# Kernel optimization log

Hardware: AMD Instinct MI355X
Metric: run time of the kernel (lower is better)

The kernel has to match this reference:

```python
import jax, jax.numpy as jnp
import numpy as np

NUM_HEADS = 4
EPS = 1e-12  # torch F.normalize eps


def _l2norm(t):
    # normalize along last axis, matching torch.nn.functional.normalize
    n = jnp.sqrt(jnp.sum(t * t, axis=-1, keepdims=True))
    return t / jnp.maximum(n, EPS)


def setup_inputs() -> dict:
    key = jax.random.key(0)
    k1, k2 = jax.random.split(key)
    B, N, C = 4, 8192, 768
    x = jax.random.normal(k1, (B, N, C), dtype=jnp.float32)
    W_qkvv = jax.random.normal(k2, (3 * C, C), dtype=jnp.float32) * (C ** -0.5)
    temperature = jnp.ones((NUM_HEADS, 1, 1), dtype=jnp.float32)
    return {"x": x, "W_qkvv": W_qkvv, "temperature": temperature}


def reference(x, W_qkvv, temperature):
    B, N, C = x.shape
    H = NUM_HEADS
    D = C // H
    # qkvv projection: [B,N,3C] -> [3,B,H,N,D]
    qkvv = (x @ W_qkvv.T).reshape(B, N, 3, H, D).transpose(2, 0, 3, 1, 4)
    q, k, v = qkvv[0], qkvv[1], qkvv[2]        # each [B,H,N,D]
    q = jnp.swapaxes(q, -2, -1)                # [B,H,D,N]
    k = jnp.swapaxes(k, -2, -1)                # [B,H,D,N]
    v = jnp.swapaxes(v, -2, -1)                # [B,H,D,N]
    q = _l2norm(q)
    k = _l2norm(k)
    # channel attention scores: [B,H,D,D], temperature broadcast per head
    attn = jnp.einsum('bhdn,bhen->bhde', q, k) * temperature[None]
    attn = jax.nn.softmax(attn, axis=-1)
    # dropout is identity in eval mode
    x_CA = jnp.einsum('bhde,bhen->bhdn', attn, v)   # [B,H,D,N]
    out = x_CA.transpose(0, 3, 1, 2).reshape(B, N, C)
    return out
```

## Files before the change

kernel.cpp:

```cpp
#include <hip/hip_runtime.h>
#include <hip/hip_bf16.h>
#include <cstddef>
#include <cstdint>

#define B_   4
#define N_   8192
#define C_   768
#define H_   4
#define D_   192
#define CQ_  2304
#define M_   32768

typedef __attribute__((ext_vector_type(8))) short short8_t;
typedef __attribute__((ext_vector_type(4))) float f32x4;

typedef const __attribute__((address_space(1))) uint gq_uint;
typedef __attribute__((address_space(3))) uint lds_uint;

__device__ inline ushort f2bf(float f){
  uint u = __float_as_uint(f);
  u += 0x7FFFu + ((u >> 16) & 1u);
  return (ushort)(u >> 16);
}
__device__ inline float bf2f(ushort u){ return __uint_as_float(((uint)u) << 16); }

__global__ __launch_bounds__(256) void cvt_bf16(const float* __restrict__ src,
                                                ushort* __restrict__ dst, int n4){
  int i = blockIdx.x * 256 + threadIdx.x;
  if (i < n4){
    float4 v = ((const float4*)src)[i];
    ushort4 o;
    o.x = f2bf(v.x); o.y = f2bf(v.y); o.z = f2bf(v.z); o.w = f2bf(v.w);
    ((ushort4*)dst)[i] = o;
  }
}

__global__ __launch_bounds__(512, 2) void gemm_qkvv(const ushort* __restrict__ A,
                                                    const ushort* __restrict__ W,
                                                    ushort* __restrict__ Cq,
                                                    float* __restrict__ norm2){
  extern __shared__ ushort lds[];
  const int t = threadIdx.x;
  const int bid = blockIdx.x;
  const int wg  = (bid & 7) * 144 + (bid >> 3);
  const int by = wg / 9, bx = wg % 9;
  const int m0 = by * 256, n0 = bx * 256;
  const int wid = t >> 6, lane = t & 63;
  const int wm = wid >> 2, wn = wid & 3;
  const int lr = lane & 15, lg = lane >> 4;
  const int srow  = lane >> 3;
  const int sslot = (lane & 7) ^ srow;

  f32x4 acc[8][4];
  #pragma unroll
  for (int i = 0; i < 8; ++i)
    #pragma unroll
    for (int j = 0; j < 4; ++j)
      acc[i][j] = (f32x4){0.f, 0.f, 0.f, 0.f};

  #define STAGE_HALF(GPTR, G0, KT, LBASE, HALF)                                 \
    do {                                                                        \
      _Pragma("unroll")                                                         \
      for (int rnd_ = 0; rnd_ < 2; ++rnd_){                                     \
        const int row_ = (HALF) * 128 + rnd_ * 64 + wid * 8;                    \
        __builtin_amdgcn_global_load_lds(                                       \
            (gq_uint*)(const void*)((GPTR) + (size_t)((G0) + row_ + srow) * 768 \
                                    + (KT) * 64 + sslot * 8),                   \
            (lds_uint*)(void*)((LBASE) + row_ * 64), 16, 0, 0);                 \
      }                                                                         \
    } while (0)

  #define RD_A(DST, MH)                                                         \
    _Pragma("unroll") for (int kk = 0; kk < 2; ++kk){                           \
      const int sl = ((kk * 4 + lg) ^ (lr & 7)) * 8;                            \
      _Pragma("unroll") for (int fm = 0; fm < 4; ++fm)                          \
        DST[kk][fm] = *(const short8_t*)(bA + ((MH)*128 + wm*64 + fm*16 + lr)*64 + sl); }

  #define RD_B(DST, NH)                                                         \
    _Pragma("unroll") for (int kk = 0; kk < 2; ++kk){                           \
      const int sl = ((kk * 4 + lg) ^ (lr & 7)) * 8;                            \
      _Pragma("unroll") for (int fl = 0; fl < 2; ++fl)                          \
        DST[kk][fl] = *(const short8_t*)(bB + ((NH)*128 + wn*32 + fl*16 + lr)*64 + sl); }

  #define MM(AR, BR, IO, JO)                                                    \
    __builtin_amdgcn_s_setprio(1);                                              \
    _Pragma("unroll") for (int kk = 0; kk < 2; ++kk)                            \
    _Pragma("unroll") for (int fm = 0; fm < 4; ++fm)                            \
    _Pragma("unroll") for (int fl = 0; fl < 2; ++fl)                            \
      acc[(IO)+fm][(JO)+fl] = __builtin_amdgcn_mfma_f32_16x16x32_bf16(          \
          AR[kk][fm], BR[kk][fl], acc[(IO)+fm][(JO)+fl], 0, 0, 0);              \
    __builtin_amdgcn_s_setprio(0);

  #define WAITP(N)                                                              \
    asm volatile("s_waitcnt vmcnt(" #N ")" ::: "memory");                       \
    __builtin_amdgcn_s_barrier();                                               \
    asm volatile("s_waitcnt lgkmcnt(0)" ::: "memory");                          \
    __builtin_amdgcn_sched_barrier(0);

  STAGE_HALF(A, m0, 0, lds,         0);
  STAGE_HALF(A, m0, 0, lds,         1);
  STAGE_HALF(W, n0, 0, lds + 16384, 0);
  STAGE_HALF(W, n0, 0, lds + 16384, 1);
  asm volatile("s_waitcnt vmcnt(0)" ::: "memory");
  __builtin_amdgcn_s_barrier();
  __builtin_amdgcn_sched_barrier(0);

  short8_t a0[2][4], a1[2][4], bf0[2][2], bf1[2][2];

  #pragma unroll 2
  for (int kt = 0; kt < 11; ++kt){
    const ushort* bA = lds + (kt & 1) * 32768;
    const ushort* bB = bA + 16384;
    ushort* nA = lds + ((kt + 1) & 1) * 32768;
    ushort* nB = nA + 16384;
    RD_A(a0, 0); RD_B(bf0, 0);
    STAGE_HALF(A, m0, kt + 1, nA, 0);
    WAITP(4);
    MM(a0, bf0, 0, 0);
    RD_A(a1, 1);
    STAGE_HALF(W, n0, kt + 1, nB, 0);
    WAITP(4);
    MM(a1, bf0, 4, 0);
    RD_B(bf1, 1);
    STAGE_HALF(A, m0, kt + 1, nA, 1);
    WAITP(4);
    MM(a1, bf1, 4, 2);
    STAGE_HALF(W, n0, kt + 1, nB, 1);
    WAITP(4);
    MM(a0, bf1, 0, 2);
  }
  {
    const ushort* bA = lds + 32768;
    const ushort* bB = bA + 16384;
    RD_A(a0, 0); RD_B(bf0, 0);
    WAITP(2);
    MM(a0, bf0, 0, 0);
    RD_A(a1, 1);
    WAITP(0);
    MM(a1, bf0, 4, 0);
    RD_B(bf1, 1);
    asm volatile("s_waitcnt lgkmcnt(0)" ::: "memory");
    __builtin_amdgcn_sched_barrier(0);
    MM(a1, bf1, 4, 2);
    MM(a0, bf1, 0, 2);
  }
  #undef STAGE_HALF
  #undef RD_A
  #undef RD_B
  #undef MM
  #undef WAITP

  #pragma unroll
  for (int i = 0; i < 8; ++i)
    #pragma unroll
    for (int j = 0; j < 4; ++j)
      #pragma unroll
      for (int r = 0; r < 4; ++r){
        int m = m0 + (i >> 2) * 128 + wm * 64 + (i & 3) * 16 + lg * 4 + r;
        int c = n0 + (j >> 1) * 128 + wn * 32 + (j & 1) * 16 + lr;
        Cq[(size_t)m * CQ_ + c] = f2bf(acc[i][j][r]);
      }

  if (bx < 6){
    const int b = m0 >> 13;
    #pragma unroll
    for (int j = 0; j < 4; ++j){
      float s = 0.f;
      #pragma unroll
      for (int i = 0; i < 8; ++i)
        #pragma unroll
        for (int r = 0; r < 4; ++r)
          s = fmaf(acc[i][j][r], acc[i][j][r], s);
      s += __shfl_xor(s, 16);
      s += __shfl_xor(s, 32);
      if (lg == 0)
        atomicAdd(&norm2[b * 1536 + n0 + (j >> 1) * 128 + wn * 32 + (j & 1) * 16 + lr], s);
    }
  }
}

__global__ __launch_bounds__(512) void gram_mfma(const ushort* __restrict__ Qk,
                                                 float* __restrict__ Sp){
  const int kc = blockIdx.x;
  const int bh = blockIdx.y;
  const int b = bh >> 2, h = bh & 3;
  __shared__ __align__(16) uint pk[2][2][3232];
  const int t = threadIdx.x;
  const int wid = t >> 6, lane = t & 63;
  const int wd = wid >> 2, we = wid & 3;
  const int lr = lane & 15, lg = lane >> 4;

  f32x4 acc[6][3];
  #pragma unroll
  for (int i = 0; i < 6; ++i)
    #pragma unroll
    for (int j = 0; j < 3; ++j)
      acc[i][j] = (f32x4){0.f, 0.f, 0.f, 0.f};

  const uint* gq = (const uint*)Qk + (size_t)b * N_ * 1152;

  uint r0[6], r1[6];
  #define GLOAD(IT)                                                             \
    _Pragma("unroll") for (int u = 0; u < 6; ++u){                              \
      int id = u*512 + t, mat = id/1536, rem = id - mat*1536;                   \
      int np = rem/96, c = rem - np*96;                                         \
      const uint* p = gq + (size_t)(kc*512 + (IT)*32 + 2*np)*1152               \
                         + (mat ? 384 + h*96 : h*96) + c;                       \
      r0[u] = p[0]; r1[u] = p[1152];                                            \
    }
  #define LWRITE(BUF)                                                           \
    _Pragma("unroll") for (int u = 0; u < 6; ++u){                              \
      int id = u*512 + t, mat = id/1536, rem = id - mat*1536;                   \
      int np = rem/96, c = rem - np*96;                                         \
      uint o0 = (r0[u] & 0xFFFFu) | (r1[u] << 16);                              \
      uint o1 = (r0[u] >> 16) | (r1[u] & 0xFFFF0000u);                          \
      *(uint2*)&pk[BUF][mat][np*202 + 2*c] = (uint2){o0, o1};                   \
    }

  GLOAD(0);
  LWRITE(0);
  __syncthreads();

  for (int it = 0; it < 16; ++it){
    const int cur = it & 1;
    if (it < 15) GLOAD(it + 1);
    union { uint u[4]; short8_t v; } af[6], bf[3];
    #pragma unroll
    for (int i = 0; i < 6; ++i){
      int d = wd * 96 + i * 16 + lr;
      #pragma unroll
      for (int p = 0; p < 4; ++p)
        af[i].u[p] = pk[cur][0][(lg*4 + p)*202 + d];
    }
    #pragma unroll
    for (int j = 0; j < 3; ++j){
      int e = we * 48 + j * 16 + lr;
      #pragma unroll
      for (int p = 0; p < 4; ++p)
        bf[j].u[p] = pk[cur][1][(lg*4 + p)*202 + e];
    }
    #pragma unroll
    for (int i = 0; i < 6; ++i)
      #pragma unroll
      for (int j = 0; j < 3; ++j)
        acc[i][j] = __builtin_amdgcn_mfma_f32_16x16x32_bf16(af[i].v, bf[j].v, acc[i][j], 0, 0, 0);
    if (it < 15) LWRITE(cur ^ 1);
    __syncthreads();
  }
  #undef GLOAD
  #undef LWRITE

  float* base = Sp + (size_t)(kc * 16 + bh) * 192 * 192;
  #pragma unroll
  for (int i = 0; i < 6; ++i)
    #pragma unroll
    for (int j = 0; j < 3; ++j)
      #pragma unroll
      for (int r = 0; r < 4; ++r){
        int d = wd * 96 + i * 16 + lg * 4 + r;
        int e = we * 48 + j * 16 + lr;
        base[(size_t)d * 192 + e] = acc[i][j][r];
      }
}

__global__ __launch_bounds__(256) void softmax_k(const float* __restrict__ Sp,
                                                 const float* __restrict__ norm2,
                                                 const float* __restrict__ temp,
                                                 ushort* __restrict__ attn){
  const int wid  = blockIdx.x * 4 + (threadIdx.x >> 6);
  const int lane = threadIdx.x & 63;
  const int bh = wid / 192, d = wid % 192;
  const int b = bh >> 2, h = bh & 3;
  const float nq = sqrtf(norm2[b*1536 + h*192 + d]);
  const float sc = temp[h] / fmaxf(nq, 1e-12f);
  const float* Sr = Sp + ((size_t)bh * 192 + d) * 192;
  float l[3];
  #pragma unroll
  for (int u = 0; u < 3; ++u){
    int e = lane + u * 64;
    float s = 0.f;
    #pragma unroll
    for (int kc = 0; kc < 16; ++kc)
      s += Sr[(size_t)kc * (16*192*192) + e];
    float nk = sqrtf(norm2[b*1536 + 768 + h*192 + e]);
    l[u] = s * sc / fmaxf(nk, 1e-12f);
  }
  float m = fmaxf(l[0], fmaxf(l[1], l[2]));
  #pragma unroll
  for (int off = 32; off; off >>= 1) m = fmaxf(m, __shfl_xor(m, off));
  float p[3], s = 0.f;
  #pragma unroll
  for (int u = 0; u < 3; ++u){ p[u] = expf(l[u] - m); s += p[u]; }
  #pragma unroll
  for (int off = 32; off; off >>= 1) s += __shfl_xor(s, off);
  float inv = 1.f / s;
  ushort* ar = attn + ((size_t)bh * 192 + d) * 192;
  #pragma unroll
  for (int u = 0; u < 3; ++u) ar[lane + u*64] = f2bf(p[u] * inv);
}

__global__ __launch_bounds__(256) void out_gemm(const ushort* __restrict__ Q,
                                                const ushort* __restrict__ attn,
                                                float* __restrict__ out){
  const int bh = blockIdx.y;
  const int b = bh >> 2, h = bh & 3;
  const int n0 = blockIdx.x * 128;
  const int t = threadIdx.x, w = t >> 6, lane = t & 63;
  const int wn = w & 1, wd = w >> 1;
  const int lr = lane & 15, lg = lane >> 4;
  f32x4 acc[4][6];
  #pragma unroll
  for (int i = 0; i < 4; ++i)
    #pragma unroll
    for (int j = 0; j < 6; ++j)
      acc[i][j] = (f32x4){0.f, 0.f, 0.f, 0.f};

  const ushort* Vbase = Q + 1536 + h * 192;
  const ushort* Abase = attn + (size_t)bh * 192 * 192;

  #pragma unroll
  for (int kk = 0; kk < 6; ++kk){
    const int e = kk * 32 + lg * 8;
    short8_t av[4], bv[6];
    #pragma unroll
    for (int f = 0; f < 4; ++f){
      int n = n0 + wn*64 + f*16 + lr;
      av[f] = *(const short8_t*)(Vbase + (size_t)(b*N_ + n) * CQ_ + e);
    }
    #pragma unroll
    for (int f = 0; f < 6; ++f){
      int d = wd*96 + f*16 + lr;
      bv[f] = *(const short8_t*)(Abase + d * 192 + e);
    }
    #pragma unroll
    for (int i = 0; i < 4; ++i)
      #pragma unroll
      for (int j = 0; j < 6; ++j)
        acc[i][j] = __builtin_amdgcn_mfma_f32_16x16x32_bf16(av[i], bv[j], acc[i][j], 0, 0, 0);
  }
  #pragma unroll
  for (int i = 0; i < 4; ++i)
    #pragma unroll
    for (int j = 0; j < 6; ++j)
      #pragma unroll
      for (int r = 0; r < 4; ++r){
        int n = n0 + wn*64 + i*16 + lg*4 + r;
        int c = h*192 + wd*96 + j*16 + lr;
        out[(size_t)(b*N_ + n) * 768 + c] = acc[i][j][r];
      }
}

extern "C" void kernel_launch(void* const* d_in, const int* in_sizes, int n_in,
                              void* d_out, int out_size, void* d_ws, size_t ws_size,
                              hipStream_t stream){
  const float* x    = (const float*)d_in[0];
  const float* Wq   = (const float*)d_in[1];
  const float* temp = (const float*)d_in[2];
  float* out = (float*)d_out;
  char* ws = (char*)d_ws;

  ushort* xb    = (ushort*)(ws + 0);
  float*  S_part= (float*)(ws + 0);
  ushort* attn  = (ushort*)(ws + 37748736);
  ushort* Wb    = (ushort*)(ws + 50331648);
  ushort* qkvv  = (ushort*)(ws + 53870592);
  float*  norm2 = (float*)(ws + 204865536);

  static_assert(sizeof(ushort) == 2, "");
  hipFuncSetAttribute((const void*)gemm_qkvv,
                      hipFuncAttributeMaxDynamicSharedMemorySize, 131072);

  hipMemsetAsync(norm2, 0, 24576, stream);

  cvt_bf16<<<6291456/256, 256, 0, stream>>>(x,  xb, 6291456);
  cvt_bf16<<<442368/256,  256, 0, stream>>>(Wq, Wb, 442368);

  gemm_qkvv<<<1152, 512, 131072, stream>>>(xb, Wb, qkvv, norm2);

  gram_mfma<<<dim3(16, 16), 512, 0, stream>>>(qkvv, S_part);
  softmax_k<<<768, 256, 0, stream>>>(S_part, norm2, temp, attn);
  out_gemm<<<dim3(64, 16), 256, 0, stream>>>(qkvv, attn, out);
}
```

Before: 239.1 us.

## Fuse fp32-to-bf16 conversion of x into the QKV GEMM A-tile staging

The separate pass that converted x to bf16 is removed. The QKV GEMM now loads fp32 x tiles into registers, packs them to bf16 with v_cvt_pk_bf16_f32, and writes them into LDS, while the weight tile still uses direct global-to-LDS loads. The norm2 memset is folded into the weight conversion kernel. This saves a full read and write of the converted x buffer and two launches. In exchange the GEMM's A-tile traffic doubles, register pressure rises, and the pipeline is restructured with new wait counts and barriers.

New measurement: 431.1 us. 1.8x slower.

```diff
diff --git a/kernel.cpp b/kernel.cpp
--- a/kernel.cpp
+++ b/kernel.cpp
@@ -25,8 +25,10 @@
 __device__ inline float bf2f(ushort u){ return __uint_as_float(((uint)u) << 16); }
 
 __global__ __launch_bounds__(256) void cvt_bf16(const float* __restrict__ src,
-                                                ushort* __restrict__ dst, int n4){
+                                                ushort* __restrict__ dst, int n4,
+                                                float* __restrict__ zbuf, int zn){
   int i = blockIdx.x * 256 + threadIdx.x;
+  if (i < zn) zbuf[i] = 0.f;
   if (i < n4){
     float4 v = ((const float4*)src)[i];
     ushort4 o;
@@ -35,7 +37,7 @@
   }
 }
 
-__global__ __launch_bounds__(512, 2) void gemm_qkvv(const ushort* __restrict__ A,
+__global__ __launch_bounds__(512, 2) void gemm_qkvv(const float* __restrict__ X,
                                                     const ushort* __restrict__ W,
                                                     ushort* __restrict__ Cq,
                                                     float* __restrict__ norm2){
@@ -58,13 +60,34 @@
     for (int j = 0; j < 4; ++j)
       acc[i][j] = (f32x4){0.f, 0.f, 0.f, 0.f};
 
-  #define STAGE_HALF(GPTR, G0, KT, LBASE, HALF)                                 \
+  #define ISSUE_A(RG, KT, HALF)                                                 \
+    _Pragma("unroll")                                                           \
+    for (int rnd_ = 0; rnd_ < 2; ++rnd_){                                       \
+      const int row_ = (HALF) * 128 + rnd_ * 64 + wid * 8 + srow;               \
+      const float* p_ = X + (size_t)(m0 + row_) * 768 + (KT) * 64 + sslot * 8;  \
+      RG[rnd_][0] = *(const float4*)p_;                                         \
+      RG[rnd_][1] = *(const float4*)(p_ + 4);                                   \
+    }
+
+  #define WRITE_A(RG, LBASE, HALF)                                              \
+    _Pragma("unroll")                                                           \
+    for (int rnd_ = 0; rnd_ < 2; ++rnd_){                                       \
+      uint q0_, q1_, q2_, q3_;                                                  \
+      asm("v_cvt_pk_bf16_f32 %0, %1, %2" : "=v"(q0_) : "v"(RG[rnd_][0].x), "v"(RG[rnd_][0].y)); \
+      asm("v_cvt_pk_bf16_f32 %0, %1, %2" : "=v"(q1_) : "v"(RG[rnd_][0].z), "v"(RG[rnd_][0].w)); \
+      asm("v_cvt_pk_bf16_f32 %0, %1, %2" : "=v"(q2_) : "v"(RG[rnd_][1].x), "v"(RG[rnd_][1].y)); \
+      asm("v_cvt_pk_bf16_f32 %0, %1, %2" : "=v"(q3_) : "v"(RG[rnd_][1].z), "v"(RG[rnd_][1].w)); \
+      const int row_ = (HALF) * 128 + rnd_ * 64 + wid * 8 + srow;               \
+      *(uint4*)((LBASE) + row_ * 64 + (lane & 7) * 8) = (uint4){q0_, q1_, q2_, q3_}; \
+    }
+
+  #define STAGE_W(KT, LBASE, HALF)                                              \
     do {                                                                        \
       _Pragma("unroll")                                                         \
       for (int rnd_ = 0; rnd_ < 2; ++rnd_){                                     \
         const int row_ = (HALF) * 128 + rnd_ * 64 + wid * 8;                    \
         __builtin_amdgcn_global_load_lds(                                       \
-            (gq_uint*)(const void*)((GPTR) + (size_t)((G0) + row_ + srow) * 768 \
+            (gq_uint*)(const void*)(W + (size_t)(n0 + row_ + srow) * 768        \
                                     + (KT) * 64 + sslot * 8),                   \
             (lds_uint*)(void*)((LBASE) + row_ * 64), 16, 0, 0);                 \
       }                                                                         \
@@ -91,21 +114,23 @@
           AR[kk][fm], BR[kk][fl], acc[(IO)+fm][(JO)+fl], 0, 0, 0);              \
     __builtin_amdgcn_s_setprio(0);
 
-  #define WAITP(N)                                                              \
-    asm volatile("s_waitcnt vmcnt(" #N ")" ::: "memory");                       \
+  #define BARRIER_LG                                                            \
     __builtin_amdgcn_s_barrier();                                               \
     asm volatile("s_waitcnt lgkmcnt(0)" ::: "memory");                          \
     __builtin_amdgcn_sched_barrier(0);
 
-  STAGE_HALF(A, m0, 0, lds,         0);
-  STAGE_HALF(A, m0, 0, lds,         1);
-  STAGE_HALF(W, n0, 0, lds + 16384, 0);
-  STAGE_HALF(W, n0, 0, lds + 16384, 1);
-  asm volatile("s_waitcnt vmcnt(0)" ::: "memory");
+  float4 fA0[2][2], fA1[2][2];
+  short8_t a0[2][4], a1[2][4], bf0[2][2], bf1[2][2];
+
+  ISSUE_A(fA0, 0, 0);
+  ISSUE_A(fA1, 0, 1);
+  STAGE_W(0, lds + 16384, 0);
+  STAGE_W(0, lds + 16384, 1);
+  WRITE_A(fA0, lds, 0);
+  WRITE_A(fA1, lds, 1);
+  asm volatile("s_waitcnt vmcnt(0) lgkmcnt(0)" ::: "memory");
   __builtin_amdgcn_s_barrier();
   __builtin_amdgcn_sched_barrier(0);
-
-  short8_t a0[2][4], a1[2][4], bf0[2][2], bf1[2][2];
 
   #pragma unroll 2
   for (int kt = 0; kt < 11; ++kt){
@@ -113,30 +138,41 @@
     const ushort* bB = bA + 16384;
     ushort* nA = lds + ((kt + 1) & 1) * 32768;
     ushort* nB = nA + 16384;
+
     RD_A(a0, 0); RD_B(bf0, 0);
-    STAGE_HALF(A, m0, kt + 1, nA, 0);
-    WAITP(4);
+    ISSUE_A(fA0, kt + 1, 0);
+    STAGE_W(kt + 1, nB, 0);
+    BARRIER_LG;
     MM(a0, bf0, 0, 0);
+
     RD_A(a1, 1);
-    STAGE_HALF(W, n0, kt + 1, nB, 0);
-    WAITP(4);
+    ISSUE_A(fA1, kt + 1, 1);
+    STAGE_W(kt + 1, nB, 1);
+    asm volatile("s_waitcnt vmcnt(12)" ::: "memory");
+    BARRIER_LG;
     MM(a1, bf0, 4, 0);
+
     RD_B(bf1, 1);
-    STAGE_HALF(A, m0, kt + 1, nA, 1);
-    WAITP(4);
+    WRITE_A(fA0, nA, 0);
+    BARRIER_LG;
     MM(a1, bf1, 4, 2);
-    STAGE_HALF(W, n0, kt + 1, nB, 1);
-    WAITP(4);
+
+    WRITE_A(fA1, nA, 1);
     MM(a0, bf1, 0, 2);
-  }
+    asm volatile("s_waitcnt lgkmcnt(0)" ::: "memory");
+    __builtin_amdgcn_s_barrier();
+    __builtin_amdgcn_sched_barrier(0);
+  }
+
   {
     const ushort* bA = lds + 32768;
     const ushort* bB = bA + 16384;
     RD_A(a0, 0); RD_B(bf0, 0);
-    WAITP(2);
+    BARRIER_LG;
     MM(a0, bf0, 0, 0);
     RD_A(a1, 1);
-    WAITP(0);
+    asm volatile("s_waitcnt vmcnt(0)" ::: "memory");
+    BARRIER_LG;
     MM(a1, bf0, 4, 0);
     RD_B(bf1, 1);
     asm volatile("s_waitcnt lgkmcnt(0)" ::: "memory");
@@ -144,11 +180,13 @@
     MM(a1, bf1, 4, 2);
     MM(a0, bf1, 0, 2);
   }
-  #undef STAGE_HALF
+  #undef ISSUE_A
+  #undef WRITE_A
+  #undef STAGE_W
   #undef RD_A
   #undef RD_B
   #undef MM
-  #undef WAITP
+  #undef BARRIER_LG
 
   #pragma unroll
   for (int i = 0; i < 8; ++i)
@@ -359,7 +397,6 @@
   float* out = (float*)d_out;
   char* ws = (char*)d_ws;
 
-  ushort* xb    = (ushort*)(ws + 0);
   float*  S_part= (float*)(ws + 0);
   ushort* attn  = (ushort*)(ws + 37748736);
   ushort* Wb    = (ushort*)(ws + 50331648);
@@ -370,12 +407,9 @@
   hipFuncSetAttribute((const void*)gemm_qkvv,
                       hipFuncAttributeMaxDynamicSharedMemorySize, 131072);
 
-  hipMemsetAsync(norm2, 0, 24576, stream);
-
-  cvt_bf16<<<6291456/256, 256, 0, stream>>>(x,  xb, 6291456);
-  cvt_bf16<<<442368/256,  256, 0, stream>>>(Wq, Wb, 442368);
-
-  gemm_qkvv<<<1152, 512, 131072, stream>>>(xb, Wb, qkvv, norm2);
+  cvt_bf16<<<442368/256, 256, 0, stream>>>(Wq, Wb, 442368, norm2, 6144);
+
+  gemm_qkvv<<<1152, 512, 131072, stream>>>(x, Wb, qkvv, norm2);
 
   gram_mfma<<<dim3(16, 16), 512, 0, stream>>>(qkvv, S_part);
   softmax_k<<<768, 256, 0, stream>>>(S_part, norm2, temp, attn);
```

## Shrink QKV GEMM tile to 128x256 with K=32 stages and fuse conversion launches

Applied to the files above, without the earlier changes.

The QKV projection GEMM moves from a 256x256 tile with K=64 steps and 128KB of LDS to a 128x256 tile with K=32 steps and 48KB of LDS. It uses a simpler two-buffer prefetch pipeline and launch bounds that allow four blocks per CU, so more blocks run at once and the grid doubles. The two fp32-to-bf16 conversion kernels and the norm2 memset are merged into one launch to cut launch overhead. The smaller tile lowers data reuse per block and needs more barriers per unit of K work.

Result: no change. 239.2 us (+0.1%).

```diff
diff --git a/kernel.cpp b/kernel.cpp
--- a/kernel.cpp
+++ b/kernel.cpp
@@ -24,157 +24,157 @@
 }
 __device__ inline float bf2f(ushort u){ return __uint_as_float(((uint)u) << 16); }
 
-__global__ __launch_bounds__(256) void cvt_bf16(const float* __restrict__ src,
-                                                ushort* __restrict__ dst, int n4){
+__global__ __launch_bounds__(256) void cvt_all(const float* __restrict__ x,
+                                               ushort* __restrict__ xb,
+                                               const float* __restrict__ Wq,
+                                               ushort* __restrict__ Wb,
+                                               float* __restrict__ norm2){
   int i = blockIdx.x * 256 + threadIdx.x;
-  if (i < n4){
-    float4 v = ((const float4*)src)[i];
+  if (i < 6144) norm2[i] = 0.f;
+  if (i < 6291456){
+    float4 v = ((const float4*)x)[i];
     ushort4 o;
     o.x = f2bf(v.x); o.y = f2bf(v.y); o.z = f2bf(v.z); o.w = f2bf(v.w);
-    ((ushort4*)dst)[i] = o;
-  }
-}
-
-__global__ __launch_bounds__(512, 2) void gemm_qkvv(const ushort* __restrict__ A,
+    ((ushort4*)xb)[i] = o;
+  } else if (i < 6291456 + 442368){
+    int j = i - 6291456;
+    float4 v = ((const float4*)Wq)[j];
+    ushort4 o;
+    o.x = f2bf(v.x); o.y = f2bf(v.y); o.z = f2bf(v.z); o.w = f2bf(v.w);
+    ((ushort4*)Wb)[j] = o;
+  }
+}
+
+__global__ __launch_bounds__(512, 4) void gemm_qkvv(const ushort* __restrict__ A,
                                                     const ushort* __restrict__ W,
                                                     ushort* __restrict__ Cq,
                                                     float* __restrict__ norm2){
   extern __shared__ ushort lds[];
   const int t = threadIdx.x;
   const int bid = blockIdx.x;
-  const int wg  = (bid & 7) * 144 + (bid >> 3);
+  const int wg  = (bid & 7) * 288 + (bid >> 3);
   const int by = wg / 9, bx = wg % 9;
-  const int m0 = by * 256, n0 = bx * 256;
+  const int m0 = by * 128, n0 = bx * 256;
   const int wid = t >> 6, lane = t & 63;
-  const int wm = wid >> 2, wn = wid & 3;
+  const int wr = wid >> 2, wc = wid & 3;
   const int lr = lane & 15, lg = lane >> 4;
-  const int srow  = lane >> 3;
-  const int sslot = (lane & 7) ^ srow;
-
-  f32x4 acc[8][4];
-  #pragma unroll
-  for (int i = 0; i < 8; ++i)
+  const int srow4  = lane >> 2;
+  const int sslot4 = (lane & 3) ^ (srow4 & 3);
+  const int slx = (lg ^ (lr & 3)) * 8;
+
+  f32x4 acc[4][4];
+  #pragma unroll
+  for (int i = 0; i < 4; ++i)
     #pragma unroll
     for (int j = 0; j < 4; ++j)
       acc[i][j] = (f32x4){0.f, 0.f, 0.f, 0.f};
 
-  #define STAGE_HALF(GPTR, G0, KT, LBASE, HALF)                                 \
-    do {                                                                        \
-      _Pragma("unroll")                                                         \
-      for (int rnd_ = 0; rnd_ < 2; ++rnd_){                                     \
-        const int row_ = (HALF) * 128 + rnd_ * 64 + wid * 8;                    \
-        __builtin_amdgcn_global_load_lds(                                       \
-            (gq_uint*)(const void*)((GPTR) + (size_t)((G0) + row_ + srow) * 768 \
-                                    + (KT) * 64 + sslot * 8),                   \
-            (lds_uint*)(void*)((LBASE) + row_ * 64), 16, 0, 0);                 \
-      }                                                                         \
-    } while (0)
-
-  #define RD_A(DST, MH)                                                         \
-    _Pragma("unroll") for (int kk = 0; kk < 2; ++kk){                           \
-      const int sl = ((kk * 4 + lg) ^ (lr & 7)) * 8;                            \
-      _Pragma("unroll") for (int fm = 0; fm < 4; ++fm)                          \
-        DST[kk][fm] = *(const short8_t*)(bA + ((MH)*128 + wm*64 + fm*16 + lr)*64 + sl); }
-
-  #define RD_B(DST, NH)                                                         \
-    _Pragma("unroll") for (int kk = 0; kk < 2; ++kk){                           \
-      const int sl = ((kk * 4 + lg) ^ (lr & 7)) * 8;                            \
-      _Pragma("unroll") for (int fl = 0; fl < 2; ++fl)                          \
-        DST[kk][fl] = *(const short8_t*)(bB + ((NH)*128 + wn*32 + fl*16 + lr)*64 + sl); }
-
-  #define MM(AR, BR, IO, JO)                                                    \
+  #define STAGE_A(KT, LBASE)                                                    \
+    __builtin_amdgcn_global_load_lds(                                           \
+        (gq_uint*)(const void*)(A + (size_t)(m0 + wid*16 + srow4) * 768         \
+                                + (KT) * 32 + sslot4 * 8),                      \
+        (lds_uint*)(void*)((LBASE) + wid * 512), 16, 0, 0);
+
+  #define STAGE_W(KT, LBASE)                                                    \
+    _Pragma("unroll")                                                           \
+    for (int r_ = 0; r_ < 2; ++r_){                                             \
+      __builtin_amdgcn_global_load_lds(                                         \
+          (gq_uint*)(const void*)(W + (size_t)(n0 + r_*128 + wid*16 + srow4) * 768 \
+                                  + (KT) * 32 + sslot4 * 8),                    \
+          (lds_uint*)(void*)((LBASE) + r_*4096 + wid * 512), 16, 0, 0);         \
+    }
+
+  #define RD_A(DST)                                                             \
+    _Pragma("unroll") for (int fm = 0; fm < 4; ++fm)                            \
+      DST[fm] = *(const short8_t*)(bA + (wr*64 + fm*16 + lr) * 32 + slx);
+
+  #define RD_B(DST)                                                             \
+    _Pragma("unroll") for (int fn = 0; fn < 4; ++fn)                            \
+      DST[fn] = *(const short8_t*)(bB + (wc*64 + fn*16 + lr) * 32 + slx);
+
+  #define MM(AR, BR)                                                            \
     __builtin_amdgcn_s_setprio(1);                                              \
-    _Pragma("unroll") for (int kk = 0; kk < 2; ++kk)                            \
     _Pragma("unroll") for (int fm = 0; fm < 4; ++fm)                            \
-    _Pragma("unroll") for (int fl = 0; fl < 2; ++fl)                            \
-      acc[(IO)+fm][(JO)+fl] = __builtin_amdgcn_mfma_f32_16x16x32_bf16(          \
-          AR[kk][fm], BR[kk][fl], acc[(IO)+fm][(JO)+fl], 0, 0, 0);              \
+    _Pragma("unroll") for (int fn = 0; fn < 4; ++fn)                            \
+      acc[fm][fn] = __builtin_amdgcn_mfma_f32_16x16x32_bf16(                    \
+          AR[fm], BR[fn], acc[fm][fn], 0, 0, 0);                                \
     __builtin_amdgcn_s_setprio(0);
 
-  #define WAITP(N)                                                              \
-    asm volatile("s_waitcnt vmcnt(" #N ")" ::: "memory");                       \
-    __builtin_amdgcn_s_barrier();                                               \
-    asm volatile("s_waitcnt lgkmcnt(0)" ::: "memory");                          \
-    __builtin_amdgcn_sched_barrier(0);
-
-  STAGE_HALF(A, m0, 0, lds,         0);
-  STAGE_HALF(A, m0, 0, lds,         1);
-  STAGE_HALF(W, n0, 0, lds + 16384, 0);
-  STAGE_HALF(W, n0, 0, lds + 16384, 1);
-  asm volatile("s_waitcnt vmcnt(0)" ::: "memory");
+  STAGE_A(0, lds);          STAGE_W(0, lds + 4096);
+  STAGE_A(1, lds + 12288);  STAGE_W(1, lds + 12288 + 4096);
+  asm volatile("s_waitcnt vmcnt(3)" ::: "memory");
   __builtin_amdgcn_s_barrier();
   __builtin_amdgcn_sched_barrier(0);
 
-  short8_t a0[2][4], a1[2][4], bf0[2][2], bf1[2][2];
+  short8_t af[4], bf[4];
 
   #pragma unroll 2
-  for (int kt = 0; kt < 11; ++kt){
-    const ushort* bA = lds + (kt & 1) * 32768;
-    const ushort* bB = bA + 16384;
-    ushort* nA = lds + ((kt + 1) & 1) * 32768;
-    ushort* nB = nA + 16384;
-    RD_A(a0, 0); RD_B(bf0, 0);
-    STAGE_HALF(A, m0, kt + 1, nA, 0);
-    WAITP(4);
-    MM(a0, bf0, 0, 0);
-    RD_A(a1, 1);
-    STAGE_HALF(W, n0, kt + 1, nB, 0);
-    WAITP(4);
-    MM(a1, bf0, 4, 0);
-    RD_B(bf1, 1);
-    STAGE_HALF(A, m0, kt + 1, nA, 1);
-    WAITP(4);
-    MM(a1, bf1, 4, 2);
-    STAGE_HALF(W, n0, kt + 1, nB, 1);
-    WAITP(4);
-    MM(a0, bf1, 0, 2);
+  for (int kt = 0; kt < 22; ++kt){
+    const ushort* bA = lds + (kt & 1) * 12288;
+    const ushort* bB = bA + 4096;
+    ushort* nA = lds + (kt & 1) * 12288;
+    RD_A(af); RD_B(bf);
+    asm volatile("s_waitcnt lgkmcnt(0)" ::: "memory");
+    __builtin_amdgcn_sched_barrier(0);
+    __builtin_amdgcn_s_barrier();
+    __builtin_amdgcn_sched_barrier(0);
+    STAGE_A(kt + 2, nA);
+    STAGE_W(kt + 2, nA + 4096);
+    MM(af, bf);
+    asm volatile("s_waitcnt vmcnt(3)" ::: "memory");
+    __builtin_amdgcn_s_barrier();
+    __builtin_amdgcn_sched_barrier(0);
   }
   {
-    const ushort* bA = lds + 32768;
-    const ushort* bB = bA + 16384;
-    RD_A(a0, 0); RD_B(bf0, 0);
-    WAITP(2);
-    MM(a0, bf0, 0, 0);
-    RD_A(a1, 1);
-    WAITP(0);
-    MM(a1, bf0, 4, 0);
-    RD_B(bf1, 1);
+    const ushort* bA = lds;
+    const ushort* bB = bA + 4096;
+    RD_A(af); RD_B(bf);
     asm volatile("s_waitcnt lgkmcnt(0)" ::: "memory");
     __builtin_amdgcn_sched_barrier(0);
-    MM(a1, bf1, 4, 2);
-    MM(a0, bf1, 0, 2);
-  }
-  #undef STAGE_HALF
+    MM(af, bf);
+    asm volatile("s_waitcnt vmcnt(0)" ::: "memory");
+    __builtin_amdgcn_s_barrier();
+    __builtin_amdgcn_sched_barrier(0);
+  }
+  {
+    const ushort* bA = lds + 12288;
+    const ushort* bB = bA + 4096;
+    RD_A(af); RD_B(bf);
+    asm volatile("s_waitcnt lgkmcnt(0)" ::: "memory");
+    __builtin_amdgcn_sched_barrier(0);
+    MM(af, bf);
+  }
+  #undef STAGE_A
+  #undef STAGE_W
   #undef RD_A
   #undef RD_B
   #undef MM
-  #undef WAITP
-
-  #pragma unroll
-  for (int i = 0; i < 8; ++i)
-    #pragma unroll
-    for (int j = 0; j < 4; ++j)
+
+  #pragma unroll
+  for (int fm = 0; fm < 4; ++fm)
+    #pragma unroll
+    for (int fn = 0; fn < 4; ++fn)
       #pragma unroll
       for (int r = 0; r < 4; ++r){
-        int m = m0 + (i >> 2) * 128 + wm * 64 + (i & 3) * 16 + lg * 4 + r;
-        int c = n0 + (j >> 1) * 128 + wn * 32 + (j & 1) * 16 + lr;
-        Cq[(size_t)m * CQ_ + c] = f2bf(acc[i][j][r]);
+        int m = m0 + wr*64 + fm*16 + lg*4 + r;
+        int c = n0 + wc*64 + fn*16 + lr;
+        Cq[(size_t)m * CQ_ + c] = f2bf(acc[fm][fn][r]);
       }
 
   if (bx < 6){
     const int b = m0 >> 13;
     #pragma unroll
-    for (int j = 0; j < 4; ++j){
+    for (int fn = 0; fn < 4; ++fn){
       float s = 0.f;
       #pragma unroll
-      for (int i = 0; i < 8; ++i)
+      for (int fm = 0; fm < 4; ++fm)
         #pragma unroll
         for (int r = 0; r < 4; ++r)
-          s = fmaf(acc[i][j][r], acc[i][j][r], s);
+          s = fmaf(acc[fm][fn][r], acc[fm][fn][r], s);
       s += __shfl_xor(s, 16);
       s += __shfl_xor(s, 32);
       if (lg == 0)
-        atomicAdd(&norm2[b * 1536 + n0 + (j >> 1) * 128 + wn * 32 + (j & 1) * 16 + lr], s);
+        atomicAdd(&norm2[b * 1536 + n0 + wc*64 + fn*16 + lr], s);
     }
   }
 }
@@ -368,14 +368,11 @@
 
   static_assert(sizeof(ushort) == 2, "");
   hipFuncSetAttribute((const void*)gemm_qkvv,
-                      hipFuncAttributeMaxDynamicSharedMemorySize, 131072);
-
-  hipMemsetAsync(norm2, 0, 24576, stream);
-
-  cvt_bf16<<<6291456/256, 256, 0, stream>>>(x,  xb, 6291456);
-  cvt_bf16<<<442368/256,  256, 0, stream>>>(Wq, Wb, 442368);
-
-  gemm_qkvv<<<1152, 512, 131072, stream>>>(xb, Wb, qkvv, norm2);
+                      hipFuncAttributeMaxDynamicSharedMemorySize, 49152);
+
+  cvt_all<<<26304, 256, 0, stream>>>(x, xb, Wq, Wb, norm2);
+
+  gemm_qkvv<<<2304, 512, 49152, stream>>>(xb, Wb, qkvv, norm2);
 
   gram_mfma<<<dim3(16, 16), 512, 0, stream>>>(qkvv, S_part);
   softmax_k<<<768, 256, 0, stream>>>(S_part, norm2, temp, attn);
```
